# Kernel optimization log

Hardware: AMD Instinct MI355X
Metric: run time of the kernel (lower is better)

Reference implementation:

```python
import jax, jax.numpy as jnp
import numpy as np

N = 100000      # num nodes
E = 600000      # num edges
DIN = 64        # input_dim
DH = 128        # hidden_dim
G = 512         # num graphs
EPS = 1e-5      # BatchNorm eps


def setup_inputs() -> dict:
    key = jax.random.key(0)
    ks = jax.random.split(key, 12)
    x = jax.random.normal(ks[0], (N, DIN), jnp.float32)
    edge_index = jax.random.randint(ks[1], (2, E), 0, N)
    batch = jnp.sort(jax.random.randint(ks[2], (N,), 0, G))

    def w(k, shape):
        return (jax.random.normal(k, shape, jnp.float32) / np.float32(np.sqrt(shape[0])))

    inp = {"x": x, "edge_index": edge_index, "batch": batch}
    inp.update(
        W1=w(ks[3], (DIN, DH)), b1=jnp.zeros((DH,), jnp.float32),
        bn1_g=jnp.ones((DH,), jnp.float32), bn1_b=jnp.zeros((DH,), jnp.float32),
        bn1_m=jax.random.normal(ks[4], (DH,), jnp.float32) * 0.1,
        bn1_v=jnp.ones((DH,), jnp.float32),
        W2=w(ks[5], (DH, DH)), b2=jnp.zeros((DH,), jnp.float32),
        bn2_g=jnp.ones((DH,), jnp.float32), bn2_b=jnp.zeros((DH,), jnp.float32),
        bn2_m=jax.random.normal(ks[6], (DH,), jnp.float32) * 0.1,
        bn2_v=jnp.ones((DH,), jnp.float32),
        W3=w(ks[7], (DH, DH)), b3=jnp.zeros((DH,), jnp.float32),
        bn3_g=jnp.ones((DH,), jnp.float32), bn3_b=jnp.zeros((DH,), jnp.float32),
        bn3_m=jax.random.normal(ks[8], (DH,), jnp.float32) * 0.1,
        bn3_v=jnp.ones((DH,), jnp.float32),
        fc1_w=w(ks[9], (DH, DH // 2)), fc1_b=jnp.zeros((DH // 2,), jnp.float32),
        fc2_w=w(ks[10], (DH // 2, 1)), fc2_b=jnp.zeros((1,), jnp.float32),
    )
    return inp


def reference(x, edge_index, batch,
              W1, b1, bn1_g, bn1_b, bn1_m, bn1_v,
              W2, b2, bn2_g, bn2_b, bn2_m, bn2_v,
              W3, b3, bn3_g, bn3_b, bn3_m, bn3_v,
              fc1_w, fc1_b, fc2_w, fc2_b):
    # --- GCN normalization with self-loops (PyG GCNConv, sym norm) ---
    loop = jnp.arange(N, dtype=edge_index.dtype)
    src = jnp.concatenate([edge_index[0], loop])  # [E+N]
    dst = jnp.concatenate([edge_index[1], loop])  # [E+N]
    deg = jax.ops.segment_sum(jnp.ones_like(dst, jnp.float32), dst, num_segments=N)
    dis = jnp.where(deg > 0, jax.lax.rsqrt(jnp.maximum(deg, 1.0)), 0.0)
    norm = (dis[src] * dis[dst])[:, None]  # [E+N, 1]

    def conv(h, W, b):
        h = h @ W
        agg = jax.ops.segment_sum(h[src] * norm, dst, num_segments=N)
        return agg + b

    def bn(h, g, bta, m, v):
        return (h - m) * jax.lax.rsqrt(v + EPS) * g + bta  # eval-mode BatchNorm1d

    # block 1 (dropout is identity in eval)
    h = jax.nn.relu(bn(conv(x, W1, b1), bn1_g, bn1_b, bn1_m, bn1_v))
    # middle residual block (num_layers=3 -> one block)
    h = jax.nn.relu(bn(conv(h, W2, b2), bn2_g, bn2_b, bn2_m, bn2_v)) + h
    # output conv block
    h = jax.nn.relu(bn(conv(h, W3, b3), bn3_g, bn3_b, bn3_m, bn3_v))

    # global mean pool over graphs
    sums = jax.ops.segment_sum(h, batch, num_segments=G)          # [G, DH]
    cnt = jax.ops.segment_sum(jnp.ones((N, 1), h.dtype), batch, num_segments=G)
    pooled = sums / jnp.maximum(cnt, 1.0)

    h = jax.nn.relu(pooled @ fc1_w + fc1_b)
    return jax.nn.sigmoid(h @ fc2_w + fc2_b)  # [G, 1]
```

## Files before the change

kernel.cpp:

```cpp
#include <hip/hip_runtime.h>
#include <math.h>

#define N_NODES 100000
#define N_EDGES 600000
#define DIN     64
#define DH      128
#define NG      512
#define EPS_BN  1e-5f
#define SCAN_TPB 256
#define N_SCAN_BLK ((N_NODES + SCAN_TPB - 1) / SCAN_TPB)

typedef unsigned short u16;
typedef unsigned long long u64;
typedef short s16x8 __attribute__((ext_vector_type(8)));
typedef float f32x4 __attribute__((ext_vector_type(4)));

__device__ __forceinline__ u16 f2bf(float x) {
    unsigned u = __builtin_bit_cast(unsigned, x);
    u += 0x7fffu + ((u >> 16) & 1u);
    return (u16)(u >> 16);
}
__device__ __forceinline__ float bf2f(u16 h) {
    unsigned u = ((unsigned)h) << 16;
    return __builtin_bit_cast(float, u);
}

__global__ __launch_bounds__(256) void deg_kernel(const int* __restrict__ dst,
                                                  float* __restrict__ deg, int E) {
    int e = blockIdx.x * blockDim.x + threadIdx.x;
    if (e < E) atomicAdd(&deg[dst[e]], 1.0f);
}

__global__ __launch_bounds__(256) void dis_kernel(const float* __restrict__ deg,
                                                  float* __restrict__ dis,
                                                  int* __restrict__ deg_i, int n) {
    int i = blockIdx.x * blockDim.x + threadIdx.x;
    if (i < n) {
        float d = deg[i];
        dis[i] = rsqrtf(d + 1.0f);
        deg_i[i] = (int)d;
    }
}

__global__ __launch_bounds__(SCAN_TPB) void scan1_kernel(const int* __restrict__ deg_i,
                                                         int* __restrict__ row_ptr,
                                                         int* __restrict__ blk, int n) {
    __shared__ int sm[SCAN_TPB];
    const int t = threadIdx.x;
    const int i = blockIdx.x * SCAN_TPB + t;
    const int v = (i < n) ? deg_i[i] : 0;
    sm[t] = v;
    __syncthreads();
#pragma unroll
    for (int off = 1; off < SCAN_TPB; off <<= 1) {
        int u = (t >= off) ? sm[t - off] : 0;
        __syncthreads();
        sm[t] += u;
        __syncthreads();
    }
    if (i < n) row_ptr[i] = sm[t] - v;
    if (t == SCAN_TPB - 1) blk[blockIdx.x] = sm[t];
}

__global__ __launch_bounds__(512) void scan2_kernel(int* __restrict__ blk,
                                                    int* __restrict__ row_ptr,
                                                    int nblk, int n) {
    __shared__ int sm[512];
    const int t = threadIdx.x;
    const int v = (t < nblk) ? blk[t] : 0;
    sm[t] = v;
    __syncthreads();
#pragma unroll
    for (int off = 1; off < 512; off <<= 1) {
        int u = (t >= off) ? sm[t - off] : 0;
        __syncthreads();
        sm[t] += u;
        __syncthreads();
    }
    if (t < nblk) blk[t] = sm[t] - v;
    if (t == nblk - 1) row_ptr[n] = sm[t];
}

__global__ __launch_bounds__(SCAN_TPB) void scan3_kernel(int* __restrict__ row_ptr,
                                                         const int* __restrict__ blk, int n) {
    const int i = blockIdx.x * SCAN_TPB + threadIdx.x;
    if (i < n) row_ptr[i] += blk[blockIdx.x];
}

__global__ __launch_bounds__(256) void build_csr_kernel(const int* __restrict__ src,
                                                        const int* __restrict__ dst,
                                                        const float* __restrict__ dis,
                                                        const int* __restrict__ row_ptr,
                                                        int* __restrict__ cursor,
                                                        u64* __restrict__ colval, int E) {
    int e = blockIdx.x * blockDim.x + threadIdx.x;
    if (e >= E) return;
    const int s = src[e];
    const int d = dst[e];
    const int p = atomicAdd(&cursor[d], 1);
    const unsigned fb = __builtin_bit_cast(unsigned, dis[s] * dis[d]);
    colval[row_ptr[d] + p] = ((u64)fb << 32) | (unsigned)s;
}

#define PREP_XCVT_BLKS 3125
#define PREP_WT1_BLKS  32
#define PREP_WT2_BLKS  64
#define PREP_WT3_BLKS  64
#define PREP_BN_BLKS   2
#define PREP_GB_BLKS   3
#define PREP_B0 PREP_XCVT_BLKS
#define PREP_B1 (PREP_B0 + PREP_WT1_BLKS)
#define PREP_B2 (PREP_B1 + PREP_WT2_BLKS)
#define PREP_B3 (PREP_B2 + PREP_WT3_BLKS)
#define PREP_B4 (PREP_B3 + PREP_BN_BLKS)
#define PREP_TOTAL (PREP_B4 + PREP_GB_BLKS)

__device__ __forceinline__ void wt_body(const float* __restrict__ W, u16* __restrict__ Wt,
                                        int K, int idx) {
    if (idx >= K * DH) return;
    int k = idx / DH, n = idx % DH;
    Wt[(long)n * K + k] = f2bf(W[idx]);
}

__global__ __launch_bounds__(256) void prep_kernel(
    const float* __restrict__ x, u16* __restrict__ xb,
    const float* __restrict__ W1, u16* __restrict__ Wt1,
    const float* __restrict__ W2, u16* __restrict__ Wt2,
    const float* __restrict__ W3, u16* __restrict__ Wt3,
    const float* b1, const float* g1, const float* bb1, const float* m1, const float* v1,
    const float* b2, const float* g2, const float* bb2, const float* m2, const float* v2,
    const float* b3, const float* g3, const float* bb3, const float* m3, const float* v3,
    float* __restrict__ sc, float* __restrict__ sh,
    const int* __restrict__ batch, int* __restrict__ gp) {
    const int b = blockIdx.x;
    const int tid = threadIdx.x;
    if (b < PREP_B0) {
        const long i = ((long)b * 256 + tid) * 8;
        const float4 a = *(const float4*)(x + i);
        const float4 c = *(const float4*)(x + i + 4);
        s16x8 o;
        o[0] = (short)f2bf(a.x); o[1] = (short)f2bf(a.y);
        o[2] = (short)f2bf(a.z); o[3] = (short)f2bf(a.w);
        o[4] = (short)f2bf(c.x); o[5] = (short)f2bf(c.y);
        o[6] = (short)f2bf(c.z); o[7] = (short)f2bf(c.w);
        *(s16x8*)(xb + i) = o;
    } else if (b < PREP_B1) {
        wt_body(W1, Wt1, DIN, (b - PREP_B0) * 256 + tid);
    } else if (b < PREP_B2) {
        wt_body(W2, Wt2, DH, (b - PREP_B1) * 256 + tid);
    } else if (b < PREP_B3) {
        wt_body(W3, Wt3, DH, (b - PREP_B2) * 256 + tid);
    } else if (b < PREP_B4) {
        const int i = (b - PREP_B3) * 256 + tid;
        if (i < 3 * DH) {
            int l = i >> 7, c = i & (DH - 1);
            const float* bc = l == 0 ? b1 : (l == 1 ? b2 : b3);
            const float* g  = l == 0 ? g1 : (l == 1 ? g2 : g3);
            const float* bb = l == 0 ? bb1 : (l == 1 ? bb2 : bb3);
            const float* m  = l == 0 ? m1 : (l == 1 ? m2 : m3);
            const float* v  = l == 0 ? v1 : (l == 1 ? v2 : v3);
            float s = g[c] * rsqrtf(v[c] + EPS_BN);
            sc[i] = s;
            sh[i] = (bc[c] - m[c]) * s + bb[c];
        }
    } else {
        const int g = (b - PREP_B4) * 256 + tid;
        if (g <= NG) {
            int lo = 0, hi = N_NODES;
            while (lo < hi) {
                int mid = (lo + hi) >> 1;
                if (batch[mid] < g) lo = mid + 1; else hi = mid;
            }
            gp[g] = lo;
        }
    }
}

template <int K>
__global__ __launch_bounds__(256) void gemm_mfma(const u16* __restrict__ A,
                                                 const u16* __restrict__ Wt,
                                                 u16* __restrict__ C,
                                                 int M) {
    const int wave = threadIdx.x >> 6;
    const int lane = threadIdx.x & 63;
    const int r16 = lane & 15;
    const int kc  = lane >> 4;
    const long row0 = (long)blockIdx.x * 64 + wave * 16;

    f32x4 acc[8];
#pragma unroll
    for (int t = 0; t < 8; ++t)
#pragma unroll
        for (int q = 0; q < 4; ++q) acc[t][q] = 0.0f;

    long arow = row0 + r16;
    if (arow >= M) arow = M - 1;
    const u16* ap = A + arow * K + kc * 8;

#pragma unroll
    for (int ks = 0; ks < K; ks += 32) {
        const s16x8 a = *(const s16x8*)(ap + ks);
#pragma unroll
        for (int t = 0; t < 8; ++t) {
            const s16x8 b = *(const s16x8*)(Wt + (long)(t * 16 + r16) * K + ks + kc * 8);
            acc[t] = __builtin_amdgcn_mfma_f32_16x16x32_bf16(a, b, acc[t], 0, 0, 0);
        }
    }

#pragma unroll
    for (int r = 0; r < 4; ++r) {
        const long row = row0 + kc * 4 + r;
        if (row < M) {
            u16* cp = C + row * DH + r16;
#pragma unroll
            for (int t = 0; t < 8; ++t) cp[t * 16] = f2bf(acc[t][r]);
        }
    }
}

template <bool RES>
__global__ __launch_bounds__(256) void agg_epi_kernel(const u16* __restrict__ H,
                                                      const int* __restrict__ row_ptr,
                                                      const u64* __restrict__ colval,
                                                      const float* __restrict__ dis,
                                                      const float* __restrict__ scl,
                                                      const float* __restrict__ shf,
                                                      u16* __restrict__ out, int n) {
    const long t = (long)blockIdx.x * blockDim.x + threadIdx.x;
    const int lane = (int)(t & 31);
    const long i = t >> 5;
    if (i >= n) return;
    const int cl = lane & 15;
    const int eh = lane >> 4;
    const int c = cl * 8;

    float acc[8] = {0, 0, 0, 0, 0, 0, 0, 0};
    if (eh == 0) {
        float d2 = dis[i];
        d2 *= d2;
        const s16x8 hv = *(const s16x8*)(H + i * DH + c);
#pragma unroll
        for (int q = 0; q < 8; ++q) acc[q] = bf2f((u16)hv[q]) * d2;
    }

    const int beg = row_ptr[i];
    const int end = row_ptr[i + 1];
    for (int e = beg + eh; e < end; e += 2) {
        const u64 cv = colval[e];
        const int s = (int)(unsigned)cv;
        const float nm = __builtin_bit_cast(float, (unsigned)(cv >> 32));
        const s16x8 v = *(const s16x8*)(H + (long)s * DH + c);
#pragma unroll
        for (int q = 0; q < 8; ++q) acc[q] = fmaf(bf2f((u16)v[q]), nm, acc[q]);
    }

#pragma unroll
    for (int q = 0; q < 8; ++q) acc[q] += __shfl_xor(acc[q], 16);

    if (eh == 0) {
        const float4 s0 = *(const float4*)(scl + c);
        const float4 s1 = *(const float4*)(scl + c + 4);
        const float4 f0 = *(const float4*)(shf + c);
        const float4 f1 = *(const float4*)(shf + c + 4);
        const float sv[8] = {s0.x, s0.y, s0.z, s0.w, s1.x, s1.y, s1.z, s1.w};
        const float fv[8] = {f0.x, f0.y, f0.z, f0.w, f1.x, f1.y, f1.z, f1.w};

        float r[8];
#pragma unroll
        for (int q = 0; q < 8; ++q) r[q] = fmaxf(fmaf(acc[q], sv[q], fv[q]), 0.0f);
        if (RES) {
            const s16x8 rv = *(const s16x8*)(out + i * DH + c);
#pragma unroll
            for (int q = 0; q < 8; ++q) r[q] += bf2f((u16)rv[q]);
        }
        s16x8 ov;
#pragma unroll
        for (int q = 0; q < 8; ++q) ov[q] = (short)f2bf(r[q]);
        *(s16x8*)(out + i * DH + c) = ov;
    }
}

__global__ __launch_bounds__(256) void pool_kernel(const u16* __restrict__ h,
                                                   const int* __restrict__ gp,
                                                   float* __restrict__ pooled) {
    const int g = blockIdx.x;
    const int t = threadIdx.x;
    const int grp = t >> 4;
    const int cl = t & 15;
    const int c = cl * 8;
    const int beg = gp[g];
    const int end = gp[g + 1];

    float acc[8] = {0, 0, 0, 0, 0, 0, 0, 0};
    for (int i = beg + grp; i < end; i += 16) {
        const s16x8 v = *(const s16x8*)(h + (long)i * DH + c);
#pragma unroll
        for (int q = 0; q < 8; ++q) acc[q] += bf2f((u16)v[q]);
    }

    __shared__ float sm[16][DH];
#pragma unroll
    for (int q = 0; q < 8; ++q) sm[grp][c + q] = acc[q];
    __syncthreads();

    if (t < DH) {
        float s = 0.0f;
#pragma unroll
        for (int r = 0; r < 16; ++r) s += sm[r][t];
        pooled[(long)g * DH + t] = s / fmaxf((float)(end - beg), 1.0f);
    }
}

__global__ __launch_bounds__(64) void head_kernel(const float* __restrict__ pooled,
                                                  const float* __restrict__ fc1w,
                                                  const float* __restrict__ fc1b,
                                                  const float* __restrict__ fc2w,
                                                  const float* __restrict__ fc2b,
                                                  float* __restrict__ out) {
    const int g = blockIdx.x;
    const int j = threadIdx.x;
    __shared__ float p[DH];
    p[j]      = pooled[(long)g * DH + j];
    p[j + 64] = pooled[(long)g * DH + 64 + j];
    __syncthreads();

    float acc = 0.0f;
#pragma unroll 4
    for (int k = 0; k < DH; ++k) acc = fmaf(p[k], fc1w[(long)k * 64 + j], acc);
    const float h1 = fmaxf(acc + fc1b[j], 0.0f);
    float v = h1 * fc2w[j];
#pragma unroll
    for (int off = 32; off > 0; off >>= 1) v += __shfl_down(v, off);
    if (j == 0) out[g] = 1.0f / (1.0f + expf(-(v + fc2b[0])));
}

extern "C" void kernel_launch(void* const* d_in, const int* in_sizes, int n_in,
                              void* d_out, int out_size, void* d_ws, size_t ws_size,
                              hipStream_t stream) {
    const float* x     = (const float*)d_in[0];
    const int*   ei    = (const int*)d_in[1];
    const int*   batch = (const int*)d_in[2];
    const float* W1 = (const float*)d_in[3];
    const float* b1 = (const float*)d_in[4];
    const float* g1 = (const float*)d_in[5];
    const float* t1 = (const float*)d_in[6];
    const float* m1 = (const float*)d_in[7];
    const float* v1 = (const float*)d_in[8];
    const float* W2 = (const float*)d_in[9];
    const float* b2 = (const float*)d_in[10];
    const float* g2 = (const float*)d_in[11];
    const float* t2 = (const float*)d_in[12];
    const float* m2 = (const float*)d_in[13];
    const float* v2 = (const float*)d_in[14];
    const float* W3 = (const float*)d_in[15];
    const float* b3 = (const float*)d_in[16];
    const float* g3 = (const float*)d_in[17];
    const float* t3 = (const float*)d_in[18];
    const float* m3 = (const float*)d_in[19];
    const float* v3 = (const float*)d_in[20];
    const float* fc1w = (const float*)d_in[21];
    const float* fc1b = (const float*)d_in[22];
    const float* fc2w = (const float*)d_in[23];
    const float* fc2b = (const float*)d_in[24];

    const int* src = ei;
    const int* dst = ei + N_EDGES;

    char* ws = (char*)d_ws;
    size_t off = 0;
    auto alloc = [&](size_t bytes) -> char* {
        char* p = ws + off;
        off = (off + bytes + 511) & ~(size_t)511;
        return p;
    };
    float* deg     = (float*)alloc((size_t)2 * N_NODES * 4);
    int*   cursor  = (int*)(deg + N_NODES);
    float* dis     = (float*)alloc((size_t)N_NODES * 4);
    int*   deg_i   = (int*)  alloc((size_t)N_NODES * 4);
    int*   row_ptr = (int*)  alloc(((size_t)N_NODES + 1) * 4);
    int*   blk     = (int*)  alloc((size_t)N_SCAN_BLK * 4);
    u64*   colval  = (u64*)  alloc((size_t)N_EDGES * 8);
    int*   gp      = (int*)  alloc((size_t)(NG + 1) * 4);
    float* pooled  = (float*)alloc((size_t)NG * DH * 4);
    float* bnsc    = (float*)alloc((size_t)3 * DH * 4);
    float* bnsh    = (float*)alloc((size_t)3 * DH * 4);
    u16*   xb      = (u16*)  alloc((size_t)N_NODES * DIN * 2);
    u16*   Wt1     = (u16*)  alloc((size_t)DH * DIN * 2);
    u16*   Wt2     = (u16*)  alloc((size_t)DH * DH * 2);
    u16*   Wt3     = (u16*)  alloc((size_t)DH * DH * 2);
    u16*   bufB    = (u16*)  alloc((size_t)N_NODES * DH * 2);
    u16*   bufA    = (u16*)  alloc((size_t)N_NODES * DH * 2);

    const int TPB = 256;
    const int gEdge  = (N_EDGES + TPB - 1) / TPB;
    const int gNode  = (N_NODES + TPB - 1) / TPB;
    const int gGemm  = (N_NODES + 63) / 64;
    const int gAgg   = (int)(((long)N_NODES * 32 + TPB - 1) / TPB);

    hipMemsetAsync(deg, 0, (size_t)2 * N_NODES * 4, stream);
    deg_kernel<<<gEdge, TPB, 0, stream>>>(dst, deg, N_EDGES);
    dis_kernel<<<gNode, TPB, 0, stream>>>(deg, dis, deg_i, N_NODES);
    scan1_kernel<<<N_SCAN_BLK, SCAN_TPB, 0, stream>>>(deg_i, row_ptr, blk, N_NODES);
    scan2_kernel<<<1, 512, 0, stream>>>(blk, row_ptr, N_SCAN_BLK, N_NODES);
    scan3_kernel<<<N_SCAN_BLK, SCAN_TPB, 0, stream>>>(row_ptr, blk, N_NODES);
    build_csr_kernel<<<gEdge, TPB, 0, stream>>>(src, dst, dis, row_ptr, cursor, colval,
                                                N_EDGES);
    prep_kernel<<<PREP_TOTAL, TPB, 0, stream>>>(x, xb, W1, Wt1, W2, Wt2, W3, Wt3,
                                                b1, g1, t1, m1, v1,
                                                b2, g2, t2, m2, v2,
                                                b3, g3, t3, m3, v3,
                                                bnsc, bnsh, batch, gp);

    gemm_mfma<DIN><<<gGemm, TPB, 0, stream>>>(xb, Wt1, bufB, N_NODES);
    agg_epi_kernel<false><<<gAgg, TPB, 0, stream>>>(bufB, row_ptr, colval, dis,
                                                    bnsc, bnsh, bufA, N_NODES);
    gemm_mfma<DH><<<gGemm, TPB, 0, stream>>>(bufA, Wt2, bufB, N_NODES);
    agg_epi_kernel<true><<<gAgg, TPB, 0, stream>>>(bufB, row_ptr, colval, dis,
                                                   bnsc + DH, bnsh + DH, bufA, N_NODES);
    gemm_mfma<DH><<<gGemm, TPB, 0, stream>>>(bufA, Wt3, bufB, N_NODES);
    agg_epi_kernel<false><<<gAgg, TPB, 0, stream>>>(bufB, row_ptr, colval, dis,
                                                    bnsc + 2 * DH, bnsh + 2 * DH, bufA,
                                                    N_NODES);

    pool_kernel<<<NG, TPB, 0, stream>>>(bufA, gp, pooled);
    head_kernel<<<NG, 64, 0, stream>>>(pooled, fc1w, fc1b, fc2w, fc2b, (float*)d_out);
}
```

Baseline: 310.3 us.

## Factor GCN norm into GEMM/epilogue scaling, slim CSR and fuse setup kernels

Applies the symmetric normalization by scaling GEMM output rows by dis[src] and the aggregate by dis[dst], so the CSR stores only 4-byte column indices instead of packed index+weight. Degree counting is merged into the prep kernel, dis computation into the scan, the third scan pass is removed by adding block offsets at use, and pooling is fused with the MLP head. This cuts kernel launches and edge-list traffic, at the cost of an extra bf16 rounding of pre-scaled features.

```diff
diff --git a/kernel.cpp b/kernel.cpp
--- a/kernel.cpp
+++ b/kernel.cpp
@@ -9,9 +9,9 @@
 #define EPS_BN  1e-5f
 #define SCAN_TPB 256
 #define N_SCAN_BLK ((N_NODES + SCAN_TPB - 1) / SCAN_TPB)
+#define G_EDGE   ((N_EDGES + 255) / 256)
 
 typedef unsigned short u16;
-typedef unsigned long long u64;
 typedef short s16x8 __attribute__((ext_vector_type(8)));
 typedef float f32x4 __attribute__((ext_vector_type(4)));
 
@@ -23,83 +23,6 @@
 __device__ __forceinline__ float bf2f(u16 h) {
     unsigned u = ((unsigned)h) << 16;
     return __builtin_bit_cast(float, u);
-}
-
-__global__ __launch_bounds__(256) void deg_kernel(const int* __restrict__ dst,
-                                                  float* __restrict__ deg, int E) {
-    int e = blockIdx.x * blockDim.x + threadIdx.x;
-    if (e < E) atomicAdd(&deg[dst[e]], 1.0f);
-}
-
-__global__ __launch_bounds__(256) void dis_kernel(const float* __restrict__ deg,
-                                                  float* __restrict__ dis,
-                                                  int* __restrict__ deg_i, int n) {
-    int i = blockIdx.x * blockDim.x + threadIdx.x;
-    if (i < n) {
-        float d = deg[i];
-        dis[i] = rsqrtf(d + 1.0f);
-        deg_i[i] = (int)d;
-    }
-}
-
-__global__ __launch_bounds__(SCAN_TPB) void scan1_kernel(const int* __restrict__ deg_i,
-                                                         int* __restrict__ row_ptr,
-                                                         int* __restrict__ blk, int n) {
-    __shared__ int sm[SCAN_TPB];
-    const int t = threadIdx.x;
-    const int i = blockIdx.x * SCAN_TPB + t;
-    const int v = (i < n) ? deg_i[i] : 0;
-    sm[t] = v;
-    __syncthreads();
-#pragma unroll
-    for (int off = 1; off < SCAN_TPB; off <<= 1) {
-        int u = (t >= off) ? sm[t - off] : 0;
-        __syncthreads();
-        sm[t] += u;
-        __syncthreads();
-    }
-    if (i < n) row_ptr[i] = sm[t] - v;
-    if (t == SCAN_TPB - 1) blk[blockIdx.x] = sm[t];
-}
-
-__global__ __launch_bounds__(512) void scan2_kernel(int* __restrict__ blk,
-                                                    int* __restrict__ row_ptr,
-                                                    int nblk, int n) {
-    __shared__ int sm[512];
-    const int t = threadIdx.x;
-    const int v = (t < nblk) ? blk[t] : 0;
-    sm[t] = v;
-    __syncthreads();
-#pragma unroll
-    for (int off = 1; off < 512; off <<= 1) {
-        int u = (t >= off) ? sm[t - off] : 0;
-        __syncthreads();
-        sm[t] += u;
-        __syncthreads();
-    }
-    if (t < nblk) blk[t] = sm[t] - v;
-    if (t == nblk - 1) row_ptr[n] = sm[t];
-}
-
-__global__ __launch_bounds__(SCAN_TPB) void scan3_kernel(int* __restrict__ row_ptr,
-                                                         const int* __restrict__ blk, int n) {
-    const int i = blockIdx.x * SCAN_TPB + threadIdx.x;
-    if (i < n) row_ptr[i] += blk[blockIdx.x];
-}
-
-__global__ __launch_bounds__(256) void build_csr_kernel(const int* __restrict__ src,
-                                                        const int* __restrict__ dst,
-                                                        const float* __restrict__ dis,
-                                                        const int* __restrict__ row_ptr,
-                                                        int* __restrict__ cursor,
-                                                        u64* __restrict__ colval, int E) {
-    int e = blockIdx.x * blockDim.x + threadIdx.x;
-    if (e >= E) return;
-    const int s = src[e];
-    const int d = dst[e];
-    const int p = atomicAdd(&cursor[d], 1);
-    const unsigned fb = __builtin_bit_cast(unsigned, dis[s] * dis[d]);
-    colval[row_ptr[d] + p] = ((u64)fb << 32) | (unsigned)s;
 }
 
 #define PREP_XCVT_BLKS 3125
@@ -108,7 +31,7 @@
 #define PREP_WT3_BLKS  64
 #define PREP_BN_BLKS   2
 #define PREP_GB_BLKS   3
-#define PREP_B0 PREP_XCVT_BLKS
+#define PREP_B0 (G_EDGE + PREP_XCVT_BLKS)
 #define PREP_B1 (PREP_B0 + PREP_WT1_BLKS)
 #define PREP_B2 (PREP_B1 + PREP_WT2_BLKS)
 #define PREP_B3 (PREP_B2 + PREP_WT3_BLKS)
@@ -122,7 +45,8 @@
     Wt[(long)n * K + k] = f2bf(W[idx]);
 }
 
-__global__ __launch_bounds__(256) void prep_kernel(
+__global__ __launch_bounds__(256) void degprep_kernel(
+    const int* __restrict__ dst, int* __restrict__ deg,
     const float* __restrict__ x, u16* __restrict__ xb,
     const float* __restrict__ W1, u16* __restrict__ Wt1,
     const float* __restrict__ W2, u16* __restrict__ Wt2,
@@ -134,8 +58,11 @@
     const int* __restrict__ batch, int* __restrict__ gp) {
     const int b = blockIdx.x;
     const int tid = threadIdx.x;
-    if (b < PREP_B0) {
-        const long i = ((long)b * 256 + tid) * 8;
+    if (b < G_EDGE) {
+        const int e = b * 256 + tid;
+        if (e < N_EDGES) atomicAdd(&deg[dst[e]], 1);
+    } else if (b < PREP_B0) {
+        const long i = ((long)(b - G_EDGE) * 256 + tid) * 8;
         const float4 a = *(const float4*)(x + i);
         const float4 c = *(const float4*)(x + i + 4);
         s16x8 o;
@@ -176,9 +103,65 @@
     }
 }
 
+__global__ __launch_bounds__(SCAN_TPB) void scan1_kernel(const int* __restrict__ deg,
+                                                         float* __restrict__ dis,
+                                                         int* __restrict__ rp,
+                                                         int* __restrict__ blk, int n) {
+    __shared__ int sm[SCAN_TPB];
+    const int t = threadIdx.x;
+    const int i = blockIdx.x * SCAN_TPB + t;
+    int v = 0;
+    if (i < n) {
+        v = deg[i];
+        dis[i] = rsqrtf((float)v + 1.0f);
+    }
+    sm[t] = v;
+    __syncthreads();
+#pragma unroll
+    for (int off = 1; off < SCAN_TPB; off <<= 1) {
+        int u = (t >= off) ? sm[t - off] : 0;
+        __syncthreads();
+        sm[t] += u;
+        __syncthreads();
+    }
+    if (i <= n) rp[i] = sm[t] - v;
+    if (t == SCAN_TPB - 1) blk[blockIdx.x] = sm[t];
+}
+
+__global__ __launch_bounds__(512) void scan2_kernel(int* __restrict__ blk, int nblk) {
+    __shared__ int sm[512];
+    const int t = threadIdx.x;
+    const int v = (t < nblk) ? blk[t] : 0;
+    sm[t] = v;
+    __syncthreads();
+#pragma unroll
+    for (int off = 1; off < 512; off <<= 1) {
+        int u = (t >= off) ? sm[t - off] : 0;
+        __syncthreads();
+        sm[t] += u;
+        __syncthreads();
+    }
+    if (t < nblk) blk[t] = sm[t] - v;
+}
+
+__global__ __launch_bounds__(256) void build_csr_kernel(const int* __restrict__ src,
+                                                        const int* __restrict__ dst,
+                                                        const int* __restrict__ rp,
+                                                        const int* __restrict__ blk,
+                                                        int* __restrict__ cursor,
+                                                        int* __restrict__ col, int E) {
+    int e = blockIdx.x * blockDim.x + threadIdx.x;
+    if (e >= E) return;
+    const int s = src[e];
+    const int d = dst[e];
+    const int p = atomicAdd(&cursor[d], 1);
+    col[rp[d] + blk[d >> 8] + p] = s;
+}
+
 template <int K>
 __global__ __launch_bounds__(256) void gemm_mfma(const u16* __restrict__ A,
                                                  const u16* __restrict__ Wt,
+                                                 const float* __restrict__ dis,
                                                  u16* __restrict__ C,
                                                  int M) {
     const int wave = threadIdx.x >> 6;
@@ -211,17 +194,19 @@
     for (int r = 0; r < 4; ++r) {
         const long row = row0 + kc * 4 + r;
         if (row < M) {
+            const float dd = dis[row];
             u16* cp = C + row * DH + r16;
 #pragma unroll
-            for (int t = 0; t < 8; ++t) cp[t * 16] = f2bf(acc[t][r]);
+            for (int t = 0; t < 8; ++t) cp[t * 16] = f2bf(acc[t][r] * dd);
         }
     }
 }
 
 template <bool RES>
 __global__ __launch_bounds__(256) void agg_epi_kernel(const u16* __restrict__ H,
-                                                      const int* __restrict__ row_ptr,
-                                                      const u64* __restrict__ colval,
+                                                      const int* __restrict__ rp,
+                                                      const int* __restrict__ blk,
+                                                      const int* __restrict__ col,
                                                       const float* __restrict__ dis,
                                                       const float* __restrict__ scl,
                                                       const float* __restrict__ shf,
@@ -236,28 +221,25 @@
 
     float acc[8] = {0, 0, 0, 0, 0, 0, 0, 0};
     if (eh == 0) {
-        float d2 = dis[i];
-        d2 *= d2;
         const s16x8 hv = *(const s16x8*)(H + i * DH + c);
 #pragma unroll
-        for (int q = 0; q < 8; ++q) acc[q] = bf2f((u16)hv[q]) * d2;
-    }
-
-    const int beg = row_ptr[i];
-    const int end = row_ptr[i + 1];
+        for (int q = 0; q < 8; ++q) acc[q] = bf2f((u16)hv[q]);
+    }
+
+    const int beg = rp[i] + blk[i >> 8];
+    const int end = rp[i + 1] + blk[(int)(i + 1) >> 8];
     for (int e = beg + eh; e < end; e += 2) {
-        const u64 cv = colval[e];
-        const int s = (int)(unsigned)cv;
-        const float nm = __builtin_bit_cast(float, (unsigned)(cv >> 32));
+        const int s = col[e];
         const s16x8 v = *(const s16x8*)(H + (long)s * DH + c);
 #pragma unroll
-        for (int q = 0; q < 8; ++q) acc[q] = fmaf(bf2f((u16)v[q]), nm, acc[q]);
+        for (int q = 0; q < 8; ++q) acc[q] += bf2f((u16)v[q]);
     }
 
 #pragma unroll
     for (int q = 0; q < 8; ++q) acc[q] += __shfl_xor(acc[q], 16);
 
     if (eh == 0) {
+        const float dd = dis[i];
         const float4 s0 = *(const float4*)(scl + c);
         const float4 s1 = *(const float4*)(scl + c + 4);
         const float4 f0 = *(const float4*)(shf + c);
@@ -267,7 +249,7 @@
 
         float r[8];
 #pragma unroll
-        for (int q = 0; q < 8; ++q) r[q] = fmaxf(fmaf(acc[q], sv[q], fv[q]), 0.0f);
+        for (int q = 0; q < 8; ++q) r[q] = fmaxf(fmaf(acc[q] * dd, sv[q], fv[q]), 0.0f);
         if (RES) {
             const s16x8 rv = *(const s16x8*)(out + i * DH + c);
 #pragma unroll
@@ -280,9 +262,13 @@
     }
 }
 
-__global__ __launch_bounds__(256) void pool_kernel(const u16* __restrict__ h,
-                                                   const int* __restrict__ gp,
-                                                   float* __restrict__ pooled) {
+__global__ __launch_bounds__(256) void pool_head_kernel(const u16* __restrict__ h,
+                                                        const int* __restrict__ gp,
+                                                        const float* __restrict__ fc1w,
+                                                        const float* __restrict__ fc1b,
+                                                        const float* __restrict__ fc2w,
+                                                        const float* __restrict__ fc2b,
+                                                        float* __restrict__ out) {
     const int g = blockIdx.x;
     const int t = threadIdx.x;
     const int grp = t >> 4;
@@ -299,6 +285,7 @@
     }
 
     __shared__ float sm[16][DH];
+    __shared__ float p[DH];
 #pragma unroll
     for (int q = 0; q < 8; ++q) sm[grp][c + q] = acc[q];
     __syncthreads();
@@ -307,31 +294,20 @@
         float s = 0.0f;
 #pragma unroll
         for (int r = 0; r < 16; ++r) s += sm[r][t];
-        pooled[(long)g * DH + t] = s / fmaxf((float)(end - beg), 1.0f);
-    }
-}
-
-__global__ __launch_bounds__(64) void head_kernel(const float* __restrict__ pooled,
-                                                  const float* __restrict__ fc1w,
-                                                  const float* __restrict__ fc1b,
-                                                  const float* __restrict__ fc2w,
-                                                  const float* __restrict__ fc2b,
-                                                  float* __restrict__ out) {
-    const int g = blockIdx.x;
-    const int j = threadIdx.x;
-    __shared__ float p[DH];
-    p[j]      = pooled[(long)g * DH + j];
-    p[j + 64] = pooled[(long)g * DH + 64 + j];
+        p[t] = s / fmaxf((float)(end - beg), 1.0f);
+    }
     __syncthreads();
 
-    float acc = 0.0f;
+    if (t < 64) {
+        float a = 0.0f;
 #pragma unroll 4
-    for (int k = 0; k < DH; ++k) acc = fmaf(p[k], fc1w[(long)k * 64 + j], acc);
-    const float h1 = fmaxf(acc + fc1b[j], 0.0f);
-    float v = h1 * fc2w[j];
-#pragma unroll
-    for (int off = 32; off > 0; off >>= 1) v += __shfl_down(v, off);
-    if (j == 0) out[g] = 1.0f / (1.0f + expf(-(v + fc2b[0])));
+        for (int k = 0; k < DH; ++k) a = fmaf(p[k], fc1w[(long)k * 64 + t], a);
+        const float h1 = fmaxf(a + fc1b[t], 0.0f);
+        float v = h1 * fc2w[t];
+#pragma unroll
+        for (int off = 32; off > 0; off >>= 1) v += __shfl_down(v, off);
+        if (t == 0) out[g] = 1.0f / (1.0f + expf(-(v + fc2b[0])));
+    }
 }
 
 extern "C" void kernel_launch(void* const* d_in, const int* in_sizes, int n_in,
@@ -373,15 +349,13 @@
         off = (off + bytes + 511) & ~(size_t)511;
         return p;
     };
-    float* deg     = (float*)alloc((size_t)2 * N_NODES * 4);
-    int*   cursor  = (int*)(deg + N_NODES);
+    int*   deg     = (int*)  alloc((size_t)2 * N_NODES * 4);
+    int*   cursor  = deg + N_NODES;
     float* dis     = (float*)alloc((size_t)N_NODES * 4);
-    int*   deg_i   = (int*)  alloc((size_t)N_NODES * 4);
-    int*   row_ptr = (int*)  alloc(((size_t)N_NODES + 1) * 4);
+    int*   rp      = (int*)  alloc(((size_t)N_NODES + 1) * 4);
     int*   blk     = (int*)  alloc((size_t)N_SCAN_BLK * 4);
-    u64*   colval  = (u64*)  alloc((size_t)N_EDGES * 8);
+    int*   col     = (int*)  alloc((size_t)N_EDGES * 4);
     int*   gp      = (int*)  alloc((size_t)(NG + 1) * 4);
-    float* pooled  = (float*)alloc((size_t)NG * DH * 4);
     float* bnsc    = (float*)alloc((size_t)3 * DH * 4);
     float* bnsh    = (float*)alloc((size_t)3 * DH * 4);
     u16*   xb      = (u16*)  alloc((size_t)N_NODES * DIN * 2);
@@ -392,36 +366,31 @@
     u16*   bufA    = (u16*)  alloc((size_t)N_NODES * DH * 2);
 
     const int TPB = 256;
-    const int gEdge  = (N_EDGES + TPB - 1) / TPB;
-    const int gNode  = (N_NODES + TPB - 1) / TPB;
-    const int gGemm  = (N_NODES + 63) / 64;
-    const int gAgg   = (int)(((long)N_NODES * 32 + TPB - 1) / TPB);
+    const int gGemm = (N_NODES + 63) / 64;
+    const int gAgg  = (int)(((long)N_NODES * 32 + TPB - 1) / TPB);
 
     hipMemsetAsync(deg, 0, (size_t)2 * N_NODES * 4, stream);
-    deg_kernel<<<gEdge, TPB, 0, stream>>>(dst, deg, N_EDGES);
-    dis_kernel<<<gNode, TPB, 0, stream>>>(deg, dis, deg_i, N_NODES);
-    scan1_kernel<<<N_SCAN_BLK, SCAN_TPB, 0, stream>>>(deg_i, row_ptr, blk, N_NODES);
-    scan2_kernel<<<1, 512, 0, stream>>>(blk, row_ptr, N_SCAN_BLK, N_NODES);
-    scan3_kernel<<<N_SCAN_BLK, SCAN_TPB, 0, stream>>>(row_ptr, blk, N_NODES);
-    build_csr_kernel<<<gEdge, TPB, 0, stream>>>(src, dst, dis, row_ptr, cursor, colval,
-                                                N_EDGES);
-    prep_kernel<<<PREP_TOTAL, TPB, 0, stream>>>(x, xb, W1, Wt1, W2, Wt2, W3, Wt3,
-                                                b1, g1, t1, m1, v1,
-                                                b2, g2, t2, m2, v2,
-                                                b3, g3, t3, m3, v3,
-                                                bnsc, bnsh, batch, gp);
-
-    gemm_mfma<DIN><<<gGemm, TPB, 0, stream>>>(xb, Wt1, bufB, N_NODES);
-    agg_epi_kernel<false><<<gAgg, TPB, 0, stream>>>(bufB, row_ptr, colval, dis,
+    degprep_kernel<<<PREP_TOTAL, TPB, 0, stream>>>(dst, deg, x, xb, W1, Wt1, W2, Wt2,
+                                                   W3, Wt3,
+                                                   b1, g1, t1, m1, v1,
+                                                   b2, g2, t2, m2, v2,
+                                                   b3, g3, t3, m3, v3,
+                                                   bnsc, bnsh, batch, gp);
+    scan1_kernel<<<N_SCAN_BLK, SCAN_TPB, 0, stream>>>(deg, dis, rp, blk, N_NODES);
+    scan2_kernel<<<1, 512, 0, stream>>>(blk, N_SCAN_BLK);
+    build_csr_kernel<<<G_EDGE, TPB, 0, stream>>>(src, dst, rp, blk, cursor, col, N_EDGES);
+
+    gemm_mfma<DIN><<<gGemm, TPB, 0, stream>>>(xb, Wt1, dis, bufB, N_NODES);
+    agg_epi_kernel<false><<<gAgg, TPB, 0, stream>>>(bufB, rp, blk, col, dis,
                                                     bnsc, bnsh, bufA, N_NODES);
-    gemm_mfma<DH><<<gGemm, TPB, 0, stream>>>(bufA, Wt2, bufB, N_NODES);
-    agg_epi_kernel<true><<<gAgg, TPB, 0, stream>>>(bufB, row_ptr, colval, dis,
+    gemm_mfma<DH><<<gGemm, TPB, 0, stream>>>(bufA, Wt2, dis, bufB, N_NODES);
+    agg_epi_kernel<true><<<gAgg, TPB, 0, stream>>>(bufB, rp, blk, col, dis,
                                                    bnsc + DH, bnsh + DH, bufA, N_NODES);
-    gemm_mfma<DH><<<gGemm, TPB, 0, stream>>>(bufA, Wt3, bufB, N_NODES);
-    agg_epi_kernel<false><<<gAgg, TPB, 0, stream>>>(bufB, row_ptr, colval, dis,
+    gemm_mfma<DH><<<gGemm, TPB, 0, stream>>>(bufA, Wt3, dis, bufB, N_NODES);
+    agg_epi_kernel<false><<<gAgg, TPB, 0, stream>>>(bufB, rp, blk, col, dis,
                                                     bnsc + 2 * DH, bnsh + 2 * DH, bufA,
                                                     N_NODES);
 
-    pool_kernel<<<NG, TPB, 0, stream>>>(bufA, gp, pooled);
-    head_kernel<<<NG, 64, 0, stream>>>(pooled, fc1w, fc1b, fc2w, fc2b, (float*)d_out);
-}
+    pool_head_kernel<<<NG, TPB, 0, stream>>>(bufA, gp, fc1w, fc1b, fc2w, fc2b,
+                                             (float*)d_out);
+}
```

Result: faster. 295.0 us (-4.9%).
